# Performance work log

Hardware: AMD Instinct MI355X
Metric: run time of the kernel (lower is better)

The kernel has to match this reference:

```python
import jax, jax.numpy as jnp
import numpy as np

D_MODEL = 1024
N_HEADS = 16
HEAD_DIM = D_MODEL // N_HEADS
BATCH = 4
SEQ = 2048


def setup_inputs() -> dict:
    key = jax.random.key(0)
    k_x, k_wqkv, k_bqkv, k_wo, k_bo = jax.random.split(key, 5)
    x = jax.random.normal(k_x, (BATCH, SEQ, D_MODEL), dtype=jnp.float32)
    # causal mask: True = masked (upper triangle, excluding diagonal)
    mask = jnp.triu(jnp.ones((SEQ, SEQ), dtype=bool), k=1)
    lim = 1.0 / np.sqrt(D_MODEL)
    w_qkv = jax.random.uniform(k_wqkv, (D_MODEL, 3 * D_MODEL), jnp.float32, -lim, lim)
    b_qkv = jax.random.uniform(k_bqkv, (3 * D_MODEL,), jnp.float32, -lim, lim)
    w_out = jax.random.uniform(k_wo, (D_MODEL, D_MODEL), jnp.float32, -lim, lim)
    b_out = jax.random.uniform(k_bo, (D_MODEL,), jnp.float32, -lim, lim)
    return {"x": x, "mask": mask, "w_qkv": w_qkv, "b_qkv": b_qkv,
            "w_out": w_out, "b_out": b_out}


def reference(x, mask, w_qkv, b_qkv, w_out, b_out):
    b, s, _ = x.shape
    scale = HEAD_DIM ** -0.5
    qkv = x @ w_qkv + b_qkv                          # [b, s, 3*d]
    qkv = qkv.reshape(b, s, 3, N_HEADS, HEAD_DIM)
    qkv = jnp.transpose(qkv, (2, 0, 3, 1, 4))        # [3, b, h, s, hd]
    q, k, v = qkv[0], qkv[1], qkv[2]
    attn = jnp.einsum('bhqd,bhkd->bhqk', q, k) * scale
    attn = jnp.where(mask, -jnp.inf, attn)
    attn = jax.nn.softmax(attn, axis=-1)
    out = jnp.einsum('bhqk,bhkd->bhqd', attn, v)     # [b, h, s, hd]
    out = jnp.transpose(out, (0, 2, 1, 3)).reshape(b, s, D_MODEL)
    return out @ w_out + b_out
```

## Files before the change

kernel.cpp:

```cpp
#include <hip/hip_runtime.h>
#include <stdint.h>

typedef unsigned short u16;
typedef __attribute__((ext_vector_type(8))) short short8;
typedef __attribute__((ext_vector_type(4))) float f32x4;
typedef __attribute__((ext_vector_type(16))) float f32x16;

#define DEV static __device__ __forceinline__

#define QSCALE 0.18033688011112042f

DEV float fast_exp2(float x) { return __builtin_amdgcn_exp2f(x); }

DEV float bf2f(u16 u) { union { uint32_t i; float f; } x; x.i = ((uint32_t)u) << 16; return x.f; }
DEV u16 f2bf(float f) {
  union { float f; uint32_t i; } x; x.f = f;
  uint32_t r = x.i + 0x7FFFu + ((x.i >> 16) & 1u);
  return (u16)(r >> 16);
}
DEV uint32_t pk_bf16(float lo, float hi) {
  uint32_t r;
  asm("v_cvt_pk_bf16_f32 %0, %1, %2" : "=v"(r) : "v"(lo), "v"(hi));
  return r;
}

DEV void async_copy16(void* lds_dst, const void* gsrc) {
  typedef __attribute__((address_space(1))) void* gp_t;
  typedef __attribute__((address_space(3))) void* lp_t;
  __builtin_amdgcn_global_load_lds((gp_t)(uintptr_t)gsrc,
                                   (lp_t)(uint32_t)(uintptr_t)lds_dst, 16, 0, 0);
}

#define SLOT_BYTES 49152

DEV void stage_slot(const u16* __restrict__ A, const u16* __restrict__ Bt,
                    int m0, int n0, int k0, uint8_t* As, uint8_t* Bs, int tid) {
#pragma unroll
  for (int i = 0; i < 4; ++i) {
    int c = i * 512 + tid;
    int r = c >> 3;
    int ks = (c & 7) ^ (r & 7);
    async_copy16(As + c * 16, A + (size_t)(m0 + r) * 1024 + k0 + ks * 8);
  }
#pragma unroll
  for (int i = 0; i < 2; ++i) {
    int c = i * 512 + tid;
    int r = c >> 3;
    int ks = (c & 7) ^ (r & 7);
    async_copy16(Bs + c * 16, Bt + (size_t)(n0 + r) * 1024 + k0 + ks * 8);
  }
}

DEV void gemm256_core(const u16* __restrict__ A, const u16* __restrict__ Bt,
                      int m0, int n0, uint8_t* lds,
                      f32x4 (&acc)[4][4], int wave, int lane, int tid) {
  const int wm = (wave >> 1) * 64, wn = (wave & 1) * 64;
#pragma unroll
  for (int mf = 0; mf < 4; ++mf)
#pragma unroll
    for (int nf = 0; nf < 4; ++nf)
      acc[mf][nf] = (f32x4){0.f, 0.f, 0.f, 0.f};

  stage_slot(A, Bt, m0, n0, 0,  lds,              lds + 32768,              tid);
  stage_slot(A, Bt, m0, n0, 64, lds + SLOT_BYTES, lds + SLOT_BYTES + 32768, tid);

  int cur = 0;
#pragma unroll 1
  for (int kt = 0; kt < 16; ++kt) {
    if (kt + 2 < 16) {
      int nxt = (cur >= 1) ? cur - 1 : 2;
      stage_slot(A, Bt, m0, n0, (kt + 2) * 64,
                 lds + nxt * SLOT_BYTES, lds + nxt * SLOT_BYTES + 32768, tid);
    }
    if (kt < 14)       asm volatile("s_waitcnt vmcnt(12)" ::: "memory");
    else if (kt == 14) asm volatile("s_waitcnt vmcnt(6)"  ::: "memory");
    else               asm volatile("s_waitcnt vmcnt(0)"  ::: "memory");
    asm volatile("s_barrier" ::: "memory");

    const uint8_t* Ab = lds + cur * SLOT_BYTES;
    const uint8_t* Bb = Ab + 32768;
#pragma unroll
    for (int kk = 0; kk < 2; ++kk) {
      short8 af[4], bfr[4];
#pragma unroll
      for (int f = 0; f < 4; ++f) {
        int ra = wm + f * 16 + (lane & 15);
        af[f]  = *(const short8*)(Ab + ra * 128 + (((kk * 4 + (lane >> 4)) ^ (ra & 7)) << 4));
      }
#pragma unroll
      for (int f = 0; f < 4; ++f) {
        int rb = wn + f * 16 + (lane & 15);
        bfr[f] = *(const short8*)(Bb + rb * 128 + (((kk * 4 + (lane >> 4)) ^ (rb & 7)) << 4));
      }
      asm volatile("s_barrier" ::: "memory");
      asm volatile("s_waitcnt lgkmcnt(0)" ::: "memory");
      __builtin_amdgcn_sched_barrier(0);
      __builtin_amdgcn_s_setprio(1);
#pragma unroll
      for (int mf = 0; mf < 4; ++mf)
#pragma unroll
        for (int nf = 0; nf < 4; ++nf)
          acc[mf][nf] = __builtin_amdgcn_mfma_f32_16x16x32_bf16(af[mf], bfr[nf],
                                                                acc[mf][nf], 0, 0, 0);
      __builtin_amdgcn_s_setprio(0);
      asm volatile("s_barrier" ::: "memory");
    }
    cur = (cur == 2) ? 0 : cur + 1;
  }
}

__global__ __launch_bounds__(512, 2) void k_gemm_qkv(
    const u16* __restrict__ X, const u16* __restrict__ WT, const float* __restrict__ bias,
    u16* __restrict__ Q, u16* __restrict__ Kv, u16* __restrict__ Vt) {
  __shared__ __attribute__((aligned(16))) uint8_t lds[3 * SLOT_BYTES];
  const int tid = threadIdx.x, lane = tid & 63, wave = tid >> 6;
  const int wm = (wave >> 1) * 64, wn = (wave & 1) * 64;
  const int m0 = blockIdx.x * 256, n0 = blockIdx.y * 128;
  f32x4 acc[4][4];
  gemm256_core(X, WT, m0, n0, lds, acc, wave, lane, tid);
#pragma unroll
  for (int nf = 0; nf < 4; ++nf) {
    int n = n0 + wn + nf * 16 + (lane & 15);
    float bv = bias[n];
    int which = n >> 10, h = (n >> 6) & 15, hd = n & 63;
    if (which == 2) {
#pragma unroll
      for (int mf = 0; mf < 4; ++mf) {
        int m = m0 + wm + mf * 16 + (lane >> 4) * 4;
        int b = m >> 11, s = m & 2047;
        u16 tmp[4];
#pragma unroll
        for (int rg = 0; rg < 4; ++rg) tmp[rg] = f2bf(acc[mf][nf][rg] + bv);
        *(uint64_t*)(Vt + ((size_t)(b * 16 + h) * 64 + hd) * 2048 + s) = *(const uint64_t*)tmp;
      }
    } else {
      u16* base = (which == 0) ? Q : Kv;
      const float mul = (which == 0) ? QSCALE : 1.0f;
#pragma unroll
      for (int mf = 0; mf < 4; ++mf)
#pragma unroll
        for (int rg = 0; rg < 4; ++rg) {
          int m = m0 + wm + mf * 16 + (lane >> 4) * 4 + rg;
          int b = m >> 11, s = m & 2047;
          base[((size_t)(b * 16 + h) * 2048 + s) * 64 + hd] = f2bf((acc[mf][nf][rg] + bv) * mul);
        }
    }
  }
}

__global__ __launch_bounds__(512, 2) void k_gemm_out(
    const u16* __restrict__ A, const u16* __restrict__ WT, const float* __restrict__ bias,
    float* __restrict__ Out) {
  __shared__ __attribute__((aligned(16))) uint8_t lds[3 * SLOT_BYTES];
  const int tid = threadIdx.x, lane = tid & 63, wave = tid >> 6;
  const int wm = (wave >> 1) * 64, wn = (wave & 1) * 64;
  const int m0 = blockIdx.x * 256, n0 = blockIdx.y * 128;
  f32x4 acc[4][4];
  gemm256_core(A, WT, m0, n0, lds, acc, wave, lane, tid);
#pragma unroll
  for (int nf = 0; nf < 4; ++nf) {
    int n = n0 + wn + nf * 16 + (lane & 15);
    float bv = bias[n];
#pragma unroll
    for (int mf = 0; mf < 4; ++mf)
#pragma unroll
      for (int rg = 0; rg < 4; ++rg) {
        int m = m0 + wm + mf * 16 + (lane >> 4) * 4 + rg;
        Out[(size_t)m * 1024 + n] = acc[mf][nf][rg] + bv;
      }
  }
}

__global__ __launch_bounds__(256) void k_cvt_x(const float* __restrict__ src,
                                               u16* __restrict__ dst, int n8) {
  int i = blockIdx.x * 256 + threadIdx.x;
  if (i >= n8) return;
  float4 a = *(const float4*)(src + (size_t)i * 8);
  float4 b = *(const float4*)(src + (size_t)i * 8 + 4);
  u16 tmp[8] = {f2bf(a.x), f2bf(a.y), f2bf(a.z), f2bf(a.w),
                f2bf(b.x), f2bf(b.y), f2bf(b.z), f2bf(b.w)};
  *(short8*)(dst + (size_t)i * 8) = *(const short8*)tmp;
}

__global__ __launch_bounds__(256) void k_transpose_f32(
    const float* __restrict__ src, u16* __restrict__ dst, int R, int C) {
  __shared__ u16 tile[64][72];
  const int tr = blockIdx.x * 64, tc = blockIdx.y * 64;
  for (int c = threadIdx.x; c < 1024; c += 256) {
    int r = c >> 4, c4 = (c & 15) * 4;
    float4 v = *(const float4*)(src + (size_t)(tr + r) * C + tc + c4);
    tile[r][c4 + 0] = f2bf(v.x); tile[r][c4 + 1] = f2bf(v.y);
    tile[r][c4 + 2] = f2bf(v.z); tile[r][c4 + 3] = f2bf(v.w);
  }
  __syncthreads();
  for (int c = threadIdx.x; c < 512; c += 256) {
    int oc = c >> 3, r8 = (c & 7) * 8;
    u16 tmp[8];
#pragma unroll
    for (int i = 0; i < 8; ++i) tmp[i] = tile[r8 + i][oc];
    *(short8*)(dst + (size_t)(tc + oc) * R + tr + r8) = *(const short8*)tmp;
  }
}

DEV void stage_tile(const u16* __restrict__ Kg, const u16* __restrict__ Vg,
                    uint8_t* kb, uint8_t* vb, int t, int tid) {
#pragma unroll
  for (int i = 0; i < 2; ++i) {
    int c = i * 256 + tid;
    int r = c >> 3;
    int ks = (c & 7) ^ (r & 7);
    async_copy16(kb + c * 16, Kg + (size_t)(t * 64 + r) * 64 + ks * 8);
    async_copy16(vb + c * 16, Vg + (size_t)r * 2048 + t * 64 + ks * 8);
  }
}

__global__ __launch_bounds__(256, 2) void k_attn(
    const u16* __restrict__ Q, const u16* __restrict__ K,
    const u16* __restrict__ Vt, u16* __restrict__ O) {
  __shared__ __attribute__((aligned(16))) uint8_t kbuf[2][8192];
  __shared__ __attribute__((aligned(16))) uint8_t vbuf[2][8192];
  const int tid = threadIdx.x;
  const int lane = tid & 63;
  const int wave = tid >> 6;
  const int q32 = lane & 31, hv = lane >> 5;
  const float NEG_INF = -__builtin_inff();

  int L = blockIdx.x;
  int bh = (L & 7) * 8 + ((L >> 3) >> 3);
  int pair = (L >> 3) & 7;
  const int b = bh >> 4, h = bh & 15;
  const size_t hb = (size_t)bh * (2048 * 64);
  const u16* Qg = Q + hb;
  const u16* Kg = K + hb;
  const u16* Vg = Vt + hb;

#pragma unroll 1
  for (int which = 0; which < 2; ++which) {
    const int s = which ? (15 - pair) : pair;
    const int nt = 2 * (s + 1);
    const int qbase = s * 128 + wave * 32;
    const int qg = qbase + q32;
    const int my_nt = ((qbase + 31) >> 6) + 1;

    short8 qf[4];
#pragma unroll
    for (int dblk = 0; dblk < 4; ++dblk)
      qf[dblk] = *(const short8*)(Qg + (size_t)qg * 64 + dblk * 16 + hv * 8);

    f32x16 oacc[2] = {};
    float mrun = NEG_INF, lrun = 0.f;

    stage_tile(Kg, Vg, kbuf[0], vbuf[0], 0, tid);
    __syncthreads();

#pragma unroll 1
    for (int t = 0; t < nt; ++t) {
      const int cur = t & 1;
      if (t + 1 < nt) stage_tile(Kg, Vg, kbuf[cur ^ 1], vbuf[cur ^ 1], t + 1, tid);

      if (t < my_nt) {
        const uint8_t* kb = kbuf[cur];
        const uint8_t* vb = vbuf[cur];

        f32x16 sa0 = {}, sa1 = {};
        __builtin_amdgcn_s_setprio(1);
#pragma unroll
        for (int dblk = 0; dblk < 4; ++dblk) {
          short8 kf0 = *(const short8*)(kb + q32 * 128 + (((dblk * 2 + hv) ^ (q32 & 7)) << 4));
          short8 kf1 = *(const short8*)(kb + (32 + q32) * 128 + (((dblk * 2 + hv) ^ (q32 & 7)) << 4));
          sa0 = __builtin_amdgcn_mfma_f32_32x32x16_bf16(kf0, qf[dblk], sa0, 0, 0, 0);
          sa1 = __builtin_amdgcn_mfma_f32_32x32x16_bf16(kf1, qf[dblk], sa1, 0, 0, 0);
        }
        __builtin_amdgcn_s_setprio(0);

        float sv[32];
#pragma unroll
        for (int r = 0; r < 16; ++r) { sv[r] = sa0[r]; sv[16 + r] = sa1[r]; }
        if (t * 64 + 63 > qbase) {
#pragma unroll
          for (int r = 0; r < 16; ++r) {
            int kl = (r & 3) + 8 * (r >> 2) + 4 * hv;
            if (t * 64 + kl > qg)      sv[r]      = NEG_INF;
            if (t * 64 + 32 + kl > qg) sv[16 + r] = NEG_INF;
          }
        }

        float mloc = fmaxf(sv[0], sv[1]);
#pragma unroll
        for (int r = 2; r < 32; ++r) mloc = fmaxf(mloc, sv[r]);
        float mtile = fmaxf(mloc, __shfl_xor(mloc, 32, 64));
        if (!__all(mtile <= mrun + 8.f)) {
          float mnew = fmaxf(mrun, mtile);
          float corr = fast_exp2(mrun - mnew);
          mrun = mnew;
          lrun *= corr;
#pragma unroll
          for (int r = 0; r < 16; ++r) { oacc[0][r] *= corr; oacc[1][r] *= corr; }
        }
        float ls = 0.f;
#pragma unroll
        for (int r = 0; r < 32; ++r) { sv[r] = fast_exp2(sv[r] - mrun); ls += sv[r]; }
        ls += __shfl_xor(ls, 32, 64);
        lrun += ls;

        __builtin_amdgcn_s_setprio(1);
#pragma unroll
        for (int ksub = 0; ksub < 2; ++ksub) {
#pragma unroll
          for (int kb2 = 0; kb2 < 2; ++kb2) {
            const int rb = ksub * 16 + kb2 * 8;
            uint32_t pA = pk_bf16(sv[rb + 0], sv[rb + 1]);
            uint32_t pB = pk_bf16(sv[rb + 2], sv[rb + 3]);
            uint32_t pC = pk_bf16(sv[rb + 4], sv[rb + 5]);
            uint32_t pD = pk_bf16(sv[rb + 6], sv[rb + 7]);
            uint32_t X = hv ? pA : pC;
            uint32_t Y = hv ? pB : pD;
            uint32_t sX = (uint32_t)__shfl_xor((int)X, 32, 64);
            uint32_t sY = (uint32_t)__shfl_xor((int)Y, 32, 64);
            union { uint32_t u[4]; short8 s8; } pu;
            pu.u[0] = hv ? sX : pA;
            pu.u[1] = hv ? sY : pB;
            pu.u[2] = hv ? pC : sX;
            pu.u[3] = hv ? pD : sY;
            const int kblk = ksub * 2 + kb2;
            short8 vf0 = *(const short8*)(vb + q32 * 128 + (((kblk * 2 + hv) ^ (q32 & 7)) << 4));
            short8 vf1 = *(const short8*)(vb + (32 + q32) * 128 + (((kblk * 2 + hv) ^ (q32 & 7)) << 4));
            oacc[0] = __builtin_amdgcn_mfma_f32_32x32x16_bf16(vf0, pu.s8, oacc[0], 0, 0, 0);
            oacc[1] = __builtin_amdgcn_mfma_f32_32x32x16_bf16(vf1, pu.s8, oacc[1], 0, 0, 0);
          }
        }
        __builtin_amdgcn_s_setprio(0);
      }

      __syncthreads();
    }

    float rl = 1.0f / lrun;
    u16* orow = O + ((size_t)(b * 2048 + qg)) * 1024 + h * 64;
#pragma unroll
    for (int dt = 0; dt < 2; ++dt)
#pragma unroll
      for (int g = 0; g < 4; ++g) {
        int dbase = dt * 32 + 8 * g + 4 * hv;
        u16 tmp[4];
#pragma unroll
        for (int j2 = 0; j2 < 4; ++j2) tmp[j2] = f2bf(oacc[dt][4 * g + j2] * rl);
        *(uint64_t*)(orow + dbase) = *(const uint64_t*)tmp;
      }
  }
}

extern "C" void kernel_launch(void* const* d_in, const int* in_sizes, int n_in,
                              void* d_out, int out_size, void* d_ws, size_t ws_size,
                              hipStream_t stream) {
  const float* x     = (const float*)d_in[0];
  const float* w_qkv = (const float*)d_in[2];
  const float* b_qkv = (const float*)d_in[3];
  const float* w_out = (const float*)d_in[4];
  const float* b_out = (const float*)d_in[5];
  float* out = (float*)d_out;
  uint8_t* ws = (uint8_t*)d_ws;

  u16* wqkvT = (u16*)(ws);
  u16* woutT = (u16*)(ws +  6291456);
  u16* Xb    = (u16*)(ws +  8388608);
  u16* Qb    = (u16*)(ws + 25165824);
  u16* Kb    = (u16*)(ws + 41943040);
  u16* Vtb   = (u16*)(ws + 58720256);
  u16* AO    = Xb;

  k_cvt_x<<<dim3(4096), 256, 0, stream>>>(x, Xb, 1048576);
  k_transpose_f32<<<dim3(16, 48), 256, 0, stream>>>(w_qkv, wqkvT, 1024, 3072);
  k_transpose_f32<<<dim3(16, 16), 256, 0, stream>>>(w_out, woutT, 1024, 1024);
  k_gemm_qkv<<<dim3(32, 24), 512, 0, stream>>>(Xb, wqkvT, b_qkv, Qb, Kb, Vtb);
  k_attn<<<dim3(512), 256, 0, stream>>>(Qb, Kb, Vtb, AO);
  k_gemm_out<<<dim3(32, 8), 512, 0, stream>>>(AO, woutT, b_out, out);
}
```

Baseline: 168.3 us.

## Restructure GEMM mainloop to double-buffered LDS with staggered fragment loads and prefetch

Replaces the triple-buffered LDS pipeline in the shared GEMM core with a double buffer. Each k-tile now issues all LDS fragment reads up front, runs the first half of the MFMAs after a partial lgkmcnt wait, and issues the next global-to-LDS prefetch into the just-consumed buffer midway through the tile. This cuts per-tile barriers from five to two and shrinks LDS per block from 144KB to 96KB. The cost is a shallower prefetch distance, since only one tile is in flight while computing, plus more live registers for the second-half fragments.

```diff
diff --git a/kernel.cpp b/kernel.cpp
--- a/kernel.cpp
+++ b/kernel.cpp
@@ -31,10 +31,12 @@
                                    (lp_t)(uint32_t)(uintptr_t)lds_dst, 16, 0, 0);
 }
 
-#define SLOT_BYTES 49152
+#define BUF_BYTES 49152
 
 DEV void stage_slot(const u16* __restrict__ A, const u16* __restrict__ Bt,
-                    int m0, int n0, int k0, uint8_t* As, uint8_t* Bs, int tid) {
+                    int m0, int n0, int k0, uint8_t* buf, int tid) {
+  uint8_t* As = buf;
+  uint8_t* Bs = buf + 32768;
 #pragma unroll
   for (int i = 0; i < 4; ++i) {
     int c = i * 512 + tid;
@@ -61,58 +63,69 @@
     for (int nf = 0; nf < 4; ++nf)
       acc[mf][nf] = (f32x4){0.f, 0.f, 0.f, 0.f};
 
-  stage_slot(A, Bt, m0, n0, 0,  lds,              lds + 32768,              tid);
-  stage_slot(A, Bt, m0, n0, 64, lds + SLOT_BYTES, lds + SLOT_BYTES + 32768, tid);
-
-  int cur = 0;
+  stage_slot(A, Bt, m0, n0, 0,  lds,             tid);
+  stage_slot(A, Bt, m0, n0, 64, lds + BUF_BYTES, tid);
+  asm volatile("s_waitcnt vmcnt(6)" ::: "memory");
+  __builtin_amdgcn_s_barrier();
+
 #pragma unroll 1
   for (int kt = 0; kt < 16; ++kt) {
-    if (kt + 2 < 16) {
-      int nxt = (cur >= 1) ? cur - 1 : 2;
-      stage_slot(A, Bt, m0, n0, (kt + 2) * 64,
-                 lds + nxt * SLOT_BYTES, lds + nxt * SLOT_BYTES + 32768, tid);
+    const uint8_t* Ab = lds + (kt & 1) * BUF_BYTES;
+    const uint8_t* Bb = Ab + 32768;
+
+    short8 a0[4], b0[4], a1[4], b1[4];
+#pragma unroll
+    for (int f = 0; f < 4; ++f) {
+      int ra = wm + f * 16 + (lane & 15);
+      int rb = wn + f * 16 + (lane & 15);
+      a0[f] = *(const short8*)(Ab + ra * 128 + (((lane >> 4) ^ (ra & 7)) << 4));
+      b0[f] = *(const short8*)(Bb + rb * 128 + (((lane >> 4) ^ (rb & 7)) << 4));
     }
-    if (kt < 14)       asm volatile("s_waitcnt vmcnt(12)" ::: "memory");
-    else if (kt == 14) asm volatile("s_waitcnt vmcnt(6)"  ::: "memory");
-    else               asm volatile("s_waitcnt vmcnt(0)"  ::: "memory");
-    asm volatile("s_barrier" ::: "memory");
-
-    const uint8_t* Ab = lds + cur * SLOT_BYTES;
-    const uint8_t* Bb = Ab + 32768;
-#pragma unroll
-    for (int kk = 0; kk < 2; ++kk) {
-      short8 af[4], bfr[4];
-#pragma unroll
-      for (int f = 0; f < 4; ++f) {
-        int ra = wm + f * 16 + (lane & 15);
-        af[f]  = *(const short8*)(Ab + ra * 128 + (((kk * 4 + (lane >> 4)) ^ (ra & 7)) << 4));
-      }
-#pragma unroll
-      for (int f = 0; f < 4; ++f) {
-        int rb = wn + f * 16 + (lane & 15);
-        bfr[f] = *(const short8*)(Bb + rb * 128 + (((kk * 4 + (lane >> 4)) ^ (rb & 7)) << 4));
-      }
-      asm volatile("s_barrier" ::: "memory");
-      asm volatile("s_waitcnt lgkmcnt(0)" ::: "memory");
-      __builtin_amdgcn_sched_barrier(0);
-      __builtin_amdgcn_s_setprio(1);
-#pragma unroll
-      for (int mf = 0; mf < 4; ++mf)
-#pragma unroll
-        for (int nf = 0; nf < 4; ++nf)
-          acc[mf][nf] = __builtin_amdgcn_mfma_f32_16x16x32_bf16(af[mf], bfr[nf],
-                                                                acc[mf][nf], 0, 0, 0);
-      __builtin_amdgcn_s_setprio(0);
-      asm volatile("s_barrier" ::: "memory");
+#pragma unroll
+    for (int f = 0; f < 4; ++f) {
+      int ra = wm + f * 16 + (lane & 15);
+      int rb = wn + f * 16 + (lane & 15);
+      a1[f] = *(const short8*)(Ab + ra * 128 + (((4 + (lane >> 4)) ^ (ra & 7)) << 4));
+      b1[f] = *(const short8*)(Bb + rb * 128 + (((4 + (lane >> 4)) ^ (rb & 7)) << 4));
     }
-    cur = (cur == 2) ? 0 : cur + 1;
+
+    asm volatile("s_waitcnt lgkmcnt(8)" ::: "memory");
+    __builtin_amdgcn_sched_barrier(0);
+    __builtin_amdgcn_s_setprio(1);
+#pragma unroll
+    for (int mf = 0; mf < 4; ++mf)
+#pragma unroll
+      for (int nf = 0; nf < 4; ++nf)
+        acc[mf][nf] = __builtin_amdgcn_mfma_f32_16x16x32_bf16(a0[mf], b0[nf],
+                                                              acc[mf][nf], 0, 0, 0);
+    __builtin_amdgcn_s_setprio(0);
+
+    asm volatile("s_waitcnt lgkmcnt(0)" ::: "memory");
+    __builtin_amdgcn_sched_barrier(0);
+    __builtin_amdgcn_s_barrier();
+
+    if (kt + 2 < 16)
+      stage_slot(A, Bt, m0, n0, (kt + 2) * 64, lds + (kt & 1) * BUF_BYTES, tid);
+
+    __builtin_amdgcn_s_setprio(1);
+#pragma unroll
+    for (int mf = 0; mf < 4; ++mf)
+#pragma unroll
+      for (int nf = 0; nf < 4; ++nf)
+        acc[mf][nf] = __builtin_amdgcn_mfma_f32_16x16x32_bf16(a1[mf], b1[nf],
+                                                              acc[mf][nf], 0, 0, 0);
+    __builtin_amdgcn_s_setprio(0);
+
+    if (kt + 2 < 16) asm volatile("s_waitcnt vmcnt(6)" ::: "memory");
+    else             asm volatile("s_waitcnt vmcnt(0)" ::: "memory");
+    __builtin_amdgcn_s_barrier();
   }
 }
 
 __global__ __launch_bounds__(512, 2) void k_gemm_qkv(
     const u16* __restrict__ X, const u16* __restrict__ WT, const float* __restrict__ bias,
     u16* __restrict__ Q, u16* __restrict__ Kv, u16* __restrict__ Vt) {
-  __shared__ __attribute__((aligned(16))) uint8_t lds[3 * SLOT_BYTES];
+  __shared__ __attribute__((aligned(16))) uint8_t lds[2 * BUF_BYTES];
   const int tid = threadIdx.x, lane = tid & 63, wave = tid >> 6;
   const int wm = (wave >> 1) * 64, wn = (wave & 1) * 64;
   const int m0 = blockIdx.x * 256, n0 = blockIdx.y * 128;
@@ -151,7 +164,7 @@
 __global__ __launch_bounds__(512, 2) void k_gemm_out(
     const u16* __restrict__ A, const u16* __restrict__ WT, const float* __restrict__ bias,
     float* __restrict__ Out) {
-  __shared__ __attribute__((aligned(16))) uint8_t lds[3 * SLOT_BYTES];
+  __shared__ __attribute__((aligned(16))) uint8_t lds[2 * BUF_BYTES];
   const int tid = threadIdx.x, lane = tid & 63, wave = tid >> 6;
   const int wm = (wave >> 1) * 64, wn = (wave & 1) * 64;
   const int m0 = blockIdx.x * 256, n0 = blockIdx.y * 128;
```

Result: faster. 160.6 us (-4.6%).
